# Optimization experiments

Hardware: AMD Instinct MI355X
Metric: run time of the kernel (lower is better)

Reference implementation:

```python
import jax, jax.numpy as jnp
import numpy as np

N_NODES = 100000
N_EDGES = 640000
HIDDEN = 128
OUT = 128


def _graph_conv(x, edge_index, W_rel, b_rel, W_root):
    # PyG GraphConv (aggr='add'):
    #   out[i] = x[i] @ W_root.T + (sum_{(j->i) in E} x[j]) @ W_rel.T + b_rel
    src, dst = edge_index[0], edge_index[1]
    agg = jax.ops.segment_sum(x[src], dst, num_segments=N_NODES)  # [N, d_in]
    return x @ W_root.T + agg @ W_rel.T + b_rel


def setup_inputs() -> dict:
    key = jax.random.key(0)
    ks = jax.random.split(key, 10)
    x = jax.random.normal(ks[0], (N_NODES, HIDDEN), dtype=jnp.float32)
    edge_index = jax.random.randint(ks[1], (2, N_EDGES), 0, N_NODES, dtype=jnp.int64)
    s = 1.0 / np.sqrt(HIDDEN)
    def w(k, o, i):
        return jax.random.normal(k, (o, i), dtype=jnp.float32) * s
    return {
        "x": x,
        "edge_index": edge_index,
        "W_rel0": w(ks[2], HIDDEN, HIDDEN), "b0": jnp.zeros((HIDDEN,), jnp.float32), "W_root0": w(ks[3], HIDDEN, HIDDEN),
        "W_rel1": w(ks[4], HIDDEN, HIDDEN), "b1": jnp.zeros((HIDDEN,), jnp.float32), "W_root1": w(ks[5], HIDDEN, HIDDEN),
        "W_rel2": w(ks[6], OUT, HIDDEN),    "b2": jnp.zeros((OUT,), jnp.float32),    "W_root2": w(ks[7], OUT, HIDDEN),
    }


def reference(x, edge_index, W_rel0, b0, W_root0, W_rel1, b1, W_root1, W_rel2, b2, W_root2):
    h = jax.nn.relu(_graph_conv(x, edge_index, W_rel0, b0, W_root0))
    h = jax.nn.relu(_graph_conv(h, edge_index, W_rel1, b1, W_root1))
    h = _graph_conv(h, edge_index, W_rel2, b2, W_root2)  # no ReLU on end_conv
    return h
```

## Files before the change

kernel.cpp:

```cpp
#include <hip/hip_runtime.h>

constexpr int HID = 128;

typedef __attribute__((ext_vector_type(8))) short bf16x8;
typedef __attribute__((ext_vector_type(4))) float f32x4;

__device__ __forceinline__ unsigned short f2bf(float f) {
    unsigned int u = __float_as_uint(f);
    u += 0x7fffu + ((u >> 16) & 1u);
    return (unsigned short)(u >> 16);
}
__device__ __forceinline__ float bf_lo(unsigned int v) { return __uint_as_float(v << 16); }
__device__ __forceinline__ float bf_hi(unsigned int v) { return __uint_as_float(v & 0xffff0000u); }

__device__ __forceinline__ void gload16(const void* g, void* l) {
    __builtin_amdgcn_global_load_lds(
        (const __attribute__((address_space(1))) void*)g,
        (__attribute__((address_space(3))) void*)l, 16, 0, 0);
}

struct PrepArgs {
    const int* dst; int* deg; int* rank; int nEdges;
    const float* ws[6]; unsigned short* wd[6];
    const float* x; unsigned short* xb; int n4;
    int histBlocks, cvtwBlocks;
};

__global__ __launch_bounds__(256) void prep_k(PrepArgs a)
{
    const int b   = blockIdx.x;
    const int tid = threadIdx.x;
    if (b < a.histBlocks) {
        const int i = b * 256 + tid;
        if (i < a.nEdges) a.rank[i] = atomicAdd(&a.deg[a.dst[i]], 1);
    } else if (b < a.histBlocks + a.cvtwBlocks) {
        const int idx   = b - a.histBlocks;
        const int which = idx >> 4;
        const int i     = (idx & 15) * 256 + tid;
        const float4 v = reinterpret_cast<const float4*>(a.ws[which])[i];
        ushort4 o;
        o.x = f2bf(v.x); o.y = f2bf(v.y); o.z = f2bf(v.z); o.w = f2bf(v.w);
        reinterpret_cast<ushort4*>(a.wd[which])[i] = o;
    } else {
        const int i = (b - a.histBlocks - a.cvtwBlocks) * 256 + tid;
        if (i >= a.n4) return;
        const float4 v = reinterpret_cast<const float4*>(a.x)[i];
        ushort4 o;
        o.x = f2bf(v.x); o.y = f2bf(v.y); o.z = f2bf(v.z); o.w = f2bf(v.w);
        reinterpret_cast<ushort4*>(a.xb)[i] = o;
    }
}

__global__ __launch_bounds__(256) void scan1_k(
    const int* __restrict__ deg, int* __restrict__ part,
    int* __restrict__ blockSums, int n)
{
    __shared__ int s[256];
    const int t = threadIdx.x;
    const int i = blockIdx.x * 1024 + t * 4;
    const int e0 = (i + 0 < n) ? deg[i + 0] : 0;
    const int e1 = (i + 1 < n) ? deg[i + 1] : 0;
    const int e2 = (i + 2 < n) ? deg[i + 2] : 0;
    const int e3 = (i + 3 < n) ? deg[i + 3] : 0;
    const int local = e0 + e1 + e2 + e3;
    s[t] = local;
    __syncthreads();
    for (int off = 1; off < 256; off <<= 1) {
        int v = 0;
        if (t >= off) v = s[t - off];
        __syncthreads();
        if (t >= off) s[t] += v;
        __syncthreads();
    }
    const int incl = s[t];
    int excl = incl - local;
    if (t == 255) blockSums[blockIdx.x] = incl;
    if (i + 0 < n) part[i + 0] = excl; excl += e0;
    if (i + 1 < n) part[i + 1] = excl; excl += e1;
    if (i + 2 < n) part[i + 2] = excl; excl += e2;
    if (i + 3 < n) part[i + 3] = excl;
}

__global__ __launch_bounds__(128) void scan2_k(int* __restrict__ blockSums, int nb)
{
    __shared__ int s[128];
    const int t = threadIdx.x;
    const int v = (t < nb) ? blockSums[t] : 0;
    s[t] = v;
    __syncthreads();
    for (int off = 1; off < 128; off <<= 1) {
        int u = 0;
        if (t >= off) u = s[t - off];
        __syncthreads();
        if (t >= off) s[t] += u;
        __syncthreads();
    }
    if (t < nb) blockSums[t] = s[t] - v;
}

__global__ __launch_bounds__(256) void scan3_k(
    const int* __restrict__ part, const int* __restrict__ blockSums,
    int* __restrict__ rowStart, int n, int nEdges)
{
    const int i = blockIdx.x * blockDim.x + threadIdx.x;
    if (i < n) rowStart[i] = part[i] + blockSums[i >> 10];
    if (i == n) rowStart[n] = nEdges;
}

__global__ __launch_bounds__(256) void fill2_k(
    const int* __restrict__ src, const int* __restrict__ dst,
    const int* __restrict__ rank, const int* __restrict__ rowStart,
    int* __restrict__ eSrc, int nEdges)
{
    const int i = blockIdx.x * blockDim.x + threadIdx.x;
    if (i < nEdges) eSrc[rowStart[dst[i]] + rank[i]] = src[i];
}

__global__ __launch_bounds__(256) void gather_agg_k(
    const unsigned short* __restrict__ feat,
    const int*            __restrict__ rowStart,
    const int*            __restrict__ eSrc,
    unsigned short*       __restrict__ agg,
    int nNodes)
{
    const int wid  = (blockIdx.x * blockDim.x + threadIdx.x) >> 6;
    const int lane = threadIdx.x & 63;
    const int g    = lane >> 4;
    const int sl   = lane & 15;
    const int node = wid * 4 + g;
    if (node >= nNodes) return;

    const int beg = rowStart[node];
    const int end = rowStart[node + 1];
    const size_t colOff = (size_t)sl * 8;
    const int gbase = g << 4;

    float acc[8];
#pragma unroll
    for (int q = 0; q < 8; ++q) acc[q] = 0.f;

    for (int base = beg; base < end; base += 16) {
        const int cnt = min(16, end - base);
        const int si = eSrc[base + min(sl, cnt - 1)];

        int j = 0;
        for (; j + 8 <= cnt; j += 8) {
            uint4 v[8];
#pragma unroll
            for (int q = 0; q < 8; ++q) {
                const int s = __shfl(si, gbase + j + q, 64);
                v[q] = *reinterpret_cast<const uint4*>(feat + (size_t)s * HID + colOff);
            }
#pragma unroll
            for (int q = 0; q < 8; ++q) {
                acc[0] += bf_lo(v[q].x); acc[1] += bf_hi(v[q].x);
                acc[2] += bf_lo(v[q].y); acc[3] += bf_hi(v[q].y);
                acc[4] += bf_lo(v[q].z); acc[5] += bf_hi(v[q].z);
                acc[6] += bf_lo(v[q].w); acc[7] += bf_hi(v[q].w);
            }
        }
        if (j + 4 <= cnt) {
            uint4 v[4];
#pragma unroll
            for (int q = 0; q < 4; ++q) {
                const int s = __shfl(si, gbase + j + q, 64);
                v[q] = *reinterpret_cast<const uint4*>(feat + (size_t)s * HID + colOff);
            }
#pragma unroll
            for (int q = 0; q < 4; ++q) {
                acc[0] += bf_lo(v[q].x); acc[1] += bf_hi(v[q].x);
                acc[2] += bf_lo(v[q].y); acc[3] += bf_hi(v[q].y);
                acc[4] += bf_lo(v[q].z); acc[5] += bf_hi(v[q].z);
                acc[6] += bf_lo(v[q].w); acc[7] += bf_hi(v[q].w);
            }
            j += 4;
        }
        if (j + 2 <= cnt) {
            uint4 v[2];
#pragma unroll
            for (int q = 0; q < 2; ++q) {
                const int s = __shfl(si, gbase + j + q, 64);
                v[q] = *reinterpret_cast<const uint4*>(feat + (size_t)s * HID + colOff);
            }
#pragma unroll
            for (int q = 0; q < 2; ++q) {
                acc[0] += bf_lo(v[q].x); acc[1] += bf_hi(v[q].x);
                acc[2] += bf_lo(v[q].y); acc[3] += bf_hi(v[q].y);
                acc[4] += bf_lo(v[q].z); acc[5] += bf_hi(v[q].z);
                acc[6] += bf_lo(v[q].w); acc[7] += bf_hi(v[q].w);
            }
            j += 2;
        }
        if (j < cnt) {
            const int s = __shfl(si, gbase + j, 64);
            const uint4 v = *reinterpret_cast<const uint4*>(feat + (size_t)s * HID + colOff);
            acc[0] += bf_lo(v.x); acc[1] += bf_hi(v.x);
            acc[2] += bf_lo(v.y); acc[3] += bf_hi(v.y);
            acc[4] += bf_lo(v.z); acc[5] += bf_hi(v.z);
            acc[6] += bf_lo(v.w); acc[7] += bf_hi(v.w);
        }
    }

    uint4 o;
    o.x = (unsigned int)f2bf(acc[0]) | ((unsigned int)f2bf(acc[1]) << 16);
    o.y = (unsigned int)f2bf(acc[2]) | ((unsigned int)f2bf(acc[3]) << 16);
    o.z = (unsigned int)f2bf(acc[4]) | ((unsigned int)f2bf(acc[5]) << 16);
    o.w = (unsigned int)f2bf(acc[6]) | ((unsigned int)f2bf(acc[7]) << 16);
    *reinterpret_cast<uint4*>(agg + (size_t)node * HID + colOff) = o;
}

__device__ __forceinline__ void stage_tile(
    const unsigned short* __restrict__ F, const unsigned short* __restrict__ Wm,
    unsigned short* XsBuf, unsigned short* WsBuf,
    int w, int stHalf, int rsub, int srcColB, int k0, int row0, int rowMax)
{
    if (w < 2) {
#pragma unroll
        for (int q = 0; q < 8; ++q) {
            const int row = stHalf * 64 + q * 8 + rsub;
            const int gr  = min(row0 + row, rowMax);
            gload16((const char*)(F + (size_t)gr * HID + k0) + srcColB,
                    XsBuf + (stHalf * 64 + q * 8) * 64);
        }
    } else {
#pragma unroll
        for (int q = 0; q < 8; ++q) {
            const int row = stHalf * 64 + q * 8 + rsub;
            gload16((const char*)(Wm + (size_t)row * HID + k0) + srcColB,
                    WsBuf + (stHalf * 64 + q * 8) * 64);
        }
    }
}

template <int MODE>
__global__ __launch_bounds__(256) void gemm_mfma_k(
    const unsigned short* __restrict__ X,
    const unsigned short* __restrict__ AGG,
    const unsigned short* __restrict__ Wroot,
    const unsigned short* __restrict__ Wrel,
    const float*          __restrict__ bias,
    void*                 __restrict__ OUTv,
    int nRows)
{
    __shared__ unsigned short Xs[2][128 * 64];
    __shared__ unsigned short Ws[2][128 * 64];

    const int tid  = threadIdx.x;
    const int lane = tid & 63;
    const int w    = tid >> 6;
    const int row0 = blockIdx.x * 128;

    const int wr = w >> 1, wc = w & 1;
    const int R0 = wr * 64, C0 = wc * 64;
    const int lr = lane & 15, lk = lane >> 4;
    const int swz = (lr & 7) << 4;

    const int rsub    = lane >> 3;
    const int srcColB = (((lane & 7) ^ rsub) << 4);
    const int stHalf  = w & 1;
    const int rowMax  = nRows - 1;

    f32x4 acc[4][4];
#pragma unroll
    for (int m = 0; m < 4; ++m)
#pragma unroll
        for (int n = 0; n < 4; ++n) acc[m][n] = f32x4{0.f, 0.f, 0.f, 0.f};

    stage_tile(X, Wroot, Xs[0], Ws[0], w, stHalf, rsub, srcColB, 0, row0, rowMax);

#pragma unroll
    for (int t = 0; t < 4; ++t) {
        const int cur = t & 1;
        if (t < 3) {
            const unsigned short* Fn = (t + 1 < 2) ? X : AGG;
            const unsigned short* Wn = (t + 1 < 2) ? Wroot : Wrel;
            stage_tile(Fn, Wn, Xs[cur ^ 1], Ws[cur ^ 1],
                       w, stHalf, rsub, srcColB, ((t + 1) & 1) * 64, row0, rowMax);
            asm volatile("s_waitcnt vmcnt(8)" ::: "memory");
        } else {
            asm volatile("s_waitcnt vmcnt(0)" ::: "memory");
        }
        __builtin_amdgcn_s_barrier();

#pragma unroll
        for (int ks = 0; ks < 2; ++ks) {
            bf16x8 af[4], bfr[4];
            const int kB = (ks * 64 + lk * 16) ^ swz;
#pragma unroll
            for (int m = 0; m < 4; ++m) {
                const int row = R0 + m * 16 + lr;
                af[m] = *reinterpret_cast<const bf16x8*>((const char*)Xs[cur] + row * 128 + kB);
            }
#pragma unroll
            for (int n = 0; n < 4; ++n) {
                const int col = C0 + n * 16 + lr;
                bfr[n] = *reinterpret_cast<const bf16x8*>((const char*)Ws[cur] + col * 128 + kB);
            }
#pragma unroll
            for (int m = 0; m < 4; ++m)
#pragma unroll
                for (int n = 0; n < 4; ++n)
                    acc[m][n] = __builtin_amdgcn_mfma_f32_16x16x32_bf16(
                        af[m], bfr[n], acc[m][n], 0, 0, 0);
        }
        if (t < 3) __builtin_amdgcn_s_barrier();
    }

    float bv[4];
#pragma unroll
    for (int n = 0; n < 4; ++n) bv[n] = bias[C0 + n * 16 + lr];

#pragma unroll
    for (int m = 0; m < 4; ++m) {
        const int rbase = row0 + R0 + m * 16 + lk * 4;
#pragma unroll
        for (int j = 0; j < 4; ++j) {
            const int r = rbase + j;
            if (r < nRows) {
#pragma unroll
                for (int n = 0; n < 4; ++n) {
                    const int col = C0 + n * 16 + lr;
                    float v = acc[m][n][j] + bv[n];
                    if (MODE == 0) {
                        v = fmaxf(v, 0.f);
                        ((unsigned short*)OUTv)[(size_t)r * HID + col] = f2bf(v);
                    } else {
                        ((float*)OUTv)[(size_t)r * HID + col] = v;
                    }
                }
            }
        }
    }
}

extern "C" void kernel_launch(void* const* d_in, const int* in_sizes, int n_in,
                              void* d_out, int out_size, void* d_ws, size_t ws_size,
                              hipStream_t stream)
{
    const float* x      = (const float*)d_in[0];
    const int*   ei     = (const int*)  d_in[1];
    const float* Wrel0  = (const float*)d_in[2];
    const float* b0     = (const float*)d_in[3];
    const float* Wroot0 = (const float*)d_in[4];
    const float* Wrel1  = (const float*)d_in[5];
    const float* b1     = (const float*)d_in[6];
    const float* Wroot1 = (const float*)d_in[7];
    const float* Wrel2  = (const float*)d_in[8];
    const float* b2     = (const float*)d_in[9];
    const float* Wroot2 = (const float*)d_in[10];

    const int nNodes = in_sizes[0] / HID;
    const int nEdges = in_sizes[1] / 2;
    const int* srcI = ei;
    const int* dstI = ei + nEdges;
    const size_t nF = (size_t)nNodes * HID;

    float* OUT = (float*)d_out;

    unsigned short* xb   = (unsigned short*)d_ws;
    unsigned short* hA   = xb + nF;
    unsigned short* hB   = hA + nF;
    unsigned short* aggb = hB + nF;
    unsigned short* wb   = aggb + nF;
    int* deg       = (int*)(wb + 6 * HID * HID);
    int* part      = deg + nNodes;
    int* rowStart  = part + nNodes;
    int* blockSums = rowStart + nNodes + 1;
    int* rank      = blockSums + 128;
    int* eSrc      = rank + nEdges;

    unsigned short* Wrel0b  = wb + 0 * HID * HID;
    unsigned short* Wroot0b = wb + 1 * HID * HID;
    unsigned short* Wrel1b  = wb + 2 * HID * HID;
    unsigned short* Wroot1b = wb + 3 * HID * HID;
    unsigned short* Wrel2b  = wb + 4 * HID * HID;
    unsigned short* Wroot2b = wb + 5 * HID * HID;

    hipMemsetAsync(deg, 0, (size_t)nNodes * sizeof(int), stream);
    PrepArgs pa;
    pa.dst = dstI; pa.deg = deg; pa.rank = rank; pa.nEdges = nEdges;
    pa.ws[0] = Wrel0;  pa.wd[0] = Wrel0b;
    pa.ws[1] = Wroot0; pa.wd[1] = Wroot0b;
    pa.ws[2] = Wrel1;  pa.wd[2] = Wrel1b;
    pa.ws[3] = Wroot1; pa.wd[3] = Wroot1b;
    pa.ws[4] = Wrel2;  pa.wd[4] = Wrel2b;
    pa.ws[5] = Wroot2; pa.wd[5] = Wroot2b;
    pa.x = x; pa.xb = xb; pa.n4 = (int)(nF / 4);
    pa.histBlocks = (nEdges + 255) / 256;
    pa.cvtwBlocks = 96;
    const int prepGrid = pa.histBlocks + pa.cvtwBlocks + (pa.n4 + 255) / 256;
    prep_k<<<prepGrid, 256, 0, stream>>>(pa);

    const int nb = (nNodes + 1023) / 1024;
    scan1_k<<<nb, 256, 0, stream>>>(deg, part, blockSums, nNodes);
    scan2_k<<<1, 128, 0, stream>>>(blockSums, nb);
    scan3_k<<<(nNodes + 256) / 256, 256, 0, stream>>>(part, blockSums, rowStart, nNodes, nEdges);
    fill2_k<<<(nEdges + 255) / 256, 256, 0, stream>>>(srcI, dstI, rank, rowStart, eSrc, nEdges);

    const int aGrid = (int)(((size_t)(nNodes + 3) / 4 * 64 + 255) / 256);
    const int gGrid = (nNodes + 127) / 128;

    gather_agg_k<<<aGrid, 256, 0, stream>>>(xb, rowStart, eSrc, aggb, nNodes);
    gemm_mfma_k<0><<<gGrid, 256, 0, stream>>>(xb, aggb, Wroot0b, Wrel0b, b0, hA, nNodes);

    gather_agg_k<<<aGrid, 256, 0, stream>>>(hA, rowStart, eSrc, aggb, nNodes);
    gemm_mfma_k<0><<<gGrid, 256, 0, stream>>>(hA, aggb, Wroot1b, Wrel1b, b1, hB, nNodes);

    gather_agg_k<<<aGrid, 256, 0, stream>>>(hB, rowStart, eSrc, aggb, nNodes);
    gemm_mfma_k<1><<<gGrid, 256, 0, stream>>>(hB, aggb, Wroot2b, Wrel2b, b2, OUT, nNodes);
}
```

Baseline: 205.2 us.

## Pad degree counters to 64 bytes and single-buffer GEMM LDS staging

Each node's degree counter now sits in its own 64-byte slot, 16 ints apart, so histogram atomics on different nodes no longer contend on the same cache line. The memset and scan reads are changed to match the stride. The GEMM drops its double-buffered LDS pipeline for a single buffer with a load, barrier, compute, barrier sequence per K chunk, halving LDS use to raise occupancy. The cost is a 16x larger memset, strided scan reads, and no overlap of global loads with MFMA work inside a block.

```diff
diff --git a/kernel.cpp b/kernel.cpp
--- a/kernel.cpp
+++ b/kernel.cpp
@@ -1,6 +1,7 @@
 #include <hip/hip_runtime.h>
 
-constexpr int HID = 128;
+constexpr int HID  = 128;
+constexpr int DEGS = 16;
 
 typedef __attribute__((ext_vector_type(8))) short bf16x8;
 typedef __attribute__((ext_vector_type(4))) float f32x4;
@@ -32,7 +33,7 @@
     const int tid = threadIdx.x;
     if (b < a.histBlocks) {
         const int i = b * 256 + tid;
-        if (i < a.nEdges) a.rank[i] = atomicAdd(&a.deg[a.dst[i]], 1);
+        if (i < a.nEdges) a.rank[i] = atomicAdd(&a.deg[(size_t)a.dst[i] * DEGS], 1);
     } else if (b < a.histBlocks + a.cvtwBlocks) {
         const int idx   = b - a.histBlocks;
         const int which = idx >> 4;
@@ -58,10 +59,10 @@
     __shared__ int s[256];
     const int t = threadIdx.x;
     const int i = blockIdx.x * 1024 + t * 4;
-    const int e0 = (i + 0 < n) ? deg[i + 0] : 0;
-    const int e1 = (i + 1 < n) ? deg[i + 1] : 0;
-    const int e2 = (i + 2 < n) ? deg[i + 2] : 0;
-    const int e3 = (i + 3 < n) ? deg[i + 3] : 0;
+    const int e0 = (i + 0 < n) ? deg[(size_t)(i + 0) * DEGS] : 0;
+    const int e1 = (i + 1 < n) ? deg[(size_t)(i + 1) * DEGS] : 0;
+    const int e2 = (i + 2 < n) ? deg[(size_t)(i + 2) * DEGS] : 0;
+    const int e3 = (i + 3 < n) ? deg[(size_t)(i + 3) * DEGS] : 0;
     const int local = e0 + e1 + e2 + e3;
     s[t] = local;
     __syncthreads();
@@ -209,29 +210,6 @@
     *reinterpret_cast<uint4*>(agg + (size_t)node * HID + colOff) = o;
 }
 
-__device__ __forceinline__ void stage_tile(
-    const unsigned short* __restrict__ F, const unsigned short* __restrict__ Wm,
-    unsigned short* XsBuf, unsigned short* WsBuf,
-    int w, int stHalf, int rsub, int srcColB, int k0, int row0, int rowMax)
-{
-    if (w < 2) {
-#pragma unroll
-        for (int q = 0; q < 8; ++q) {
-            const int row = stHalf * 64 + q * 8 + rsub;
-            const int gr  = min(row0 + row, rowMax);
-            gload16((const char*)(F + (size_t)gr * HID + k0) + srcColB,
-                    XsBuf + (stHalf * 64 + q * 8) * 64);
-        }
-    } else {
-#pragma unroll
-        for (int q = 0; q < 8; ++q) {
-            const int row = stHalf * 64 + q * 8 + rsub;
-            gload16((const char*)(Wm + (size_t)row * HID + k0) + srcColB,
-                    WsBuf + (stHalf * 64 + q * 8) * 64);
-        }
-    }
-}
-
 template <int MODE>
 __global__ __launch_bounds__(256) void gemm_mfma_k(
     const unsigned short* __restrict__ X,
@@ -242,8 +220,8 @@
     void*                 __restrict__ OUTv,
     int nRows)
 {
-    __shared__ unsigned short Xs[2][128 * 64];
-    __shared__ unsigned short Ws[2][128 * 64];
+    __shared__ unsigned short Xs[128 * 64];
+    __shared__ unsigned short Ws[128 * 64];
 
     const int tid  = threadIdx.x;
     const int lane = tid & 63;
@@ -266,44 +244,54 @@
 #pragma unroll
         for (int n = 0; n < 4; ++n) acc[m][n] = f32x4{0.f, 0.f, 0.f, 0.f};
 
-    stage_tile(X, Wroot, Xs[0], Ws[0], w, stHalf, rsub, srcColB, 0, row0, rowMax);
-
-#pragma unroll
-    for (int t = 0; t < 4; ++t) {
-        const int cur = t & 1;
-        if (t < 3) {
-            const unsigned short* Fn = (t + 1 < 2) ? X : AGG;
-            const unsigned short* Wn = (t + 1 < 2) ? Wroot : Wrel;
-            stage_tile(Fn, Wn, Xs[cur ^ 1], Ws[cur ^ 1],
-                       w, stHalf, rsub, srcColB, ((t + 1) & 1) * 64, row0, rowMax);
-            asm volatile("s_waitcnt vmcnt(8)" ::: "memory");
-        } else {
-            asm volatile("s_waitcnt vmcnt(0)" ::: "memory");
-        }
-        __builtin_amdgcn_s_barrier();
-
-#pragma unroll
-        for (int ks = 0; ks < 2; ++ks) {
-            bf16x8 af[4], bfr[4];
-            const int kB = (ks * 64 + lk * 16) ^ swz;
-#pragma unroll
-            for (int m = 0; m < 4; ++m) {
-                const int row = R0 + m * 16 + lr;
-                af[m] = *reinterpret_cast<const bf16x8*>((const char*)Xs[cur] + row * 128 + kB);
-            }
-#pragma unroll
-            for (int n = 0; n < 4; ++n) {
-                const int col = C0 + n * 16 + lr;
-                bfr[n] = *reinterpret_cast<const bf16x8*>((const char*)Ws[cur] + col * 128 + kB);
-            }
-#pragma unroll
-            for (int m = 0; m < 4; ++m)
-#pragma unroll
-                for (int n = 0; n < 4; ++n)
-                    acc[m][n] = __builtin_amdgcn_mfma_f32_16x16x32_bf16(
-                        af[m], bfr[n], acc[m][n], 0, 0, 0);
-        }
-        if (t < 3) __builtin_amdgcn_s_barrier();
+#pragma unroll
+    for (int half = 0; half < 2; ++half) {
+        const unsigned short* F  = half ? AGG  : X;
+        const unsigned short* Wm = half ? Wrel : Wroot;
+#pragma unroll
+        for (int c = 0; c < 2; ++c) {
+            const int k0 = c * 64;
+            if (w < 2) {
+#pragma unroll
+                for (int q = 0; q < 8; ++q) {
+                    const int row = stHalf * 64 + q * 8 + rsub;
+                    const int gr  = min(row0 + row, rowMax);
+                    gload16((const char*)(F + (size_t)gr * HID + k0) + srcColB,
+                            Xs + (stHalf * 64 + q * 8) * 64);
+                }
+            } else {
+#pragma unroll
+                for (int q = 0; q < 8; ++q) {
+                    const int row = stHalf * 64 + q * 8 + rsub;
+                    gload16((const char*)(Wm + (size_t)row * HID + k0) + srcColB,
+                            Ws + (stHalf * 64 + q * 8) * 64);
+                }
+            }
+            __syncthreads();
+
+#pragma unroll
+            for (int ks = 0; ks < 2; ++ks) {
+                bf16x8 af[4], bfr[4];
+                const int kB = (ks * 64 + lk * 16) ^ swz;
+#pragma unroll
+                for (int m = 0; m < 4; ++m) {
+                    const int row = R0 + m * 16 + lr;
+                    af[m] = *reinterpret_cast<const bf16x8*>((const char*)Xs + row * 128 + kB);
+                }
+#pragma unroll
+                for (int n = 0; n < 4; ++n) {
+                    const int col = C0 + n * 16 + lr;
+                    bfr[n] = *reinterpret_cast<const bf16x8*>((const char*)Ws + col * 128 + kB);
+                }
+#pragma unroll
+                for (int m = 0; m < 4; ++m)
+#pragma unroll
+                    for (int n = 0; n < 4; ++n)
+                        acc[m][n] = __builtin_amdgcn_mfma_f32_16x16x32_bf16(
+                            af[m], bfr[n], acc[m][n], 0, 0, 0);
+            }
+            __syncthreads();
+        }
     }
 
     float bv[4];
@@ -363,7 +351,7 @@
     unsigned short* aggb = hB + nF;
     unsigned short* wb   = aggb + nF;
     int* deg       = (int*)(wb + 6 * HID * HID);
-    int* part      = deg + nNodes;
+    int* part      = deg + (size_t)nNodes * DEGS;
     int* rowStart  = part + nNodes;
     int* blockSums = rowStart + nNodes + 1;
     int* rank      = blockSums + 128;
@@ -376,7 +364,7 @@
     unsigned short* Wrel2b  = wb + 4 * HID * HID;
     unsigned short* Wroot2b = wb + 5 * HID * HID;
 
-    hipMemsetAsync(deg, 0, (size_t)nNodes * sizeof(int), stream);
+    hipMemsetAsync(deg, 0, (size_t)nNodes * DEGS * sizeof(int), stream);
     PrepArgs pa;
     pa.dst = dstI; pa.deg = deg; pa.rank = rank; pa.nEdges = nEdges;
     pa.ws[0] = Wrel0;  pa.wd[0] = Wrel0b;
```

After: 209.0 us. About the same (+1.9%).
